# Optimization experiments

Measured on AMD Instinct MI355X. Metric: run time of the kernel, lower is better.

## Reference

```python
import jax, jax.numpy as jnp
import numpy as np

N_MOL, N_ATOM, DEG = 32, 128, 32
N = N_MOL * N_ATOM          # 4096 real atoms (no blanks)
P = N * DEG                 # 131072 pairs
N_SENS = 20
SOFT_MIN, SOFT_MAX, HARD_MAX = 0.7, 5.0, 7.5
N_IN, N_OUT, N_HIST = 2, 3, 3
NF1 = 20                    # hipnn1 n_features
NF0 = 2 * NF1               # hipnn0 n_features (doubled in __init__)
NG = 4 * NF1                # gate logits width of InteractLayer W
N_ATOM_LAYERS = 3
NIN0 = 2 + N_HIST           # one-hot over {1,8} + x_h channels


def setup_inputs():
    rng = np.random.default_rng(0)
    species = 1 + 7 * rng.integers(0, 2, size=(N_MOL, N_ATOM))  # values in {1,8}, all nonblank
    base = np.repeat(np.arange(N), DEG)
    local = base % N_ATOM
    neigh = (local + 1 + rng.integers(0, N_ATOM - 1, size=P)) % N_ATOM  # neighbor != self
    pair_second = (base // N_ATOM) * N_ATOM + neigh                     # same-molecule pairs
    key = jax.random.key(0)
    ks = jax.random.split(key, 20)
    g = lambda i, shape, s=0.1: jax.random.normal(ks[i], shape, dtype=jnp.float32) * s
    return {
        "species": jnp.asarray(species, jnp.int32),
        "coordinates": jax.random.uniform(ks[0], (N_MOL, N_ATOM, 3), jnp.float32, 0.0, 6.0),
        "x_h": g(1, (N_MOL, N_ATOM, N_HIST)),
        "x_raw": g(2, (N_MOL, N_ATOM, N_IN)),
        "pair_first": jnp.asarray(base, jnp.int32),
        "pair_second": jnp.asarray(pair_second, jnp.int32),
        "h0_int_w": g(3, (N_SENS, NIN0, NF0)),
        "h0_self_w": g(4, (NIN0, NF0)),
        "h0_self_b": g(5, (NF0,)),
        "h0_aw": g(6, (N_ATOM_LAYERS, NF0, NF0)),
        "h0_ab": g(7, (N_ATOM_LAYERS, NF0)),
        "h1_int_w": g(8, (N_SENS, 1, NF1)),
        "h1_self_w": g(9, (1, NF1)),
        "h1_self_b": g(10, (NF1,)),
        "h1_aw": g(11, (N_ATOM_LAYERS, NF1, NF1)),
        "h1_ab": g(12, (N_ATOM_LAYERS, NF1)),
        "W_int_w": g(13, (N_SENS, NF0, NG)),
        "W_self_w": g(14, (NF0, NG)),
        "W_self_b": g(15, (NG,)),
        "pw0": g(16, (NIN0, 1)),
        "pw1": g(17, (NF1, 1)),
        "pb1": g(18, (1,)),
    }


def _sensitivity(d):
    # inverse-distance gaussian sensitivities with smooth hard cutoff
    mu = jnp.linspace(1.0 / SOFT_MAX, 1.0 / SOFT_MIN, N_SENS)
    sigma = (1.0 / SOFT_MIN - 1.0 / SOFT_MAX) / N_SENS
    sense = jnp.exp(-0.5 * jnp.square((1.0 / d[:, None] - mu) / sigma))
    cut = jnp.where(d < HARD_MAX, jnp.square(jnp.cos(jnp.pi * d / (2.0 * HARD_MAX))), 0.0)
    return sense * cut[:, None]                                     # (P, n_sens)


def _interact(x, sense, pf, ps, int_w, self_w, self_b):
    # gather neighbor features, weight by sensitivities, scatter-add to center atom
    msg = sense[:, :, None] * x[ps][:, None, :]                     # (P, ns, fin)
    env = jax.ops.segment_sum(msg, pf, num_segments=N)              # (N, ns, fin)
    ns, fin, fout = int_w.shape
    return env.reshape(N, ns * fin) @ int_w.reshape(ns * fin, fout) + x @ self_w + self_b


def _hipnn(x, sense, pf, ps, int_w, self_w, self_b, aw, ab):
    y = jax.nn.softplus(_interact(x, sense, pf, ps, int_w, self_w, self_b))
    for i in range(aw.shape[0]):
        y = jax.nn.softplus(y @ aw[i] + ab[i])
    return x, y   # (input features, final block features)


def _forward(coordinates, x_h, x_raw,
             h0_int_w, h0_self_w, h0_self_b, h0_aw, h0_ab,
             h1_int_w, h1_self_w, h1_self_b, h1_aw, h1_ab,
             W_int_w, W_self_w, W_self_b, pw0, pw1, pb1,
             species, pair_first, pair_second):
    enc = (species.reshape(-1)[:, None] == jnp.array([1, 8])).astype(jnp.float32)  # OneHotSpecies
    coord = coordinates.reshape(-1, 3)
    diff = coord[pair_first] - coord[pair_second]
    d = jnp.sqrt(jnp.sum(diff * diff, axis=-1) + 1e-12)
    sense = _sensitivity(d)
    ind_f = jnp.concatenate([enc, x_h.reshape(N, N_HIST)], axis=1)  # (N, 5)
    f0_in, f0_out = _hipnn(ind_f, sense, pair_first, pair_second,
                           h0_int_w, h0_self_w, h0_self_b, h0_aw, h0_ab)
    c_t, h_t = f0_out[:, : NF0 // 2], f0_out[:, NF0 // 2:]

    def onestep(x_in, h_t, c_t):
        x_t = _hipnn(x_in, sense, pair_first, pair_second,
                     h1_int_w, h1_self_w, h1_self_b, h1_aw, h1_ab)[1]
        tmp = _interact(jnp.concatenate([x_t, h_t], axis=-1), sense,
                        pair_first, pair_second, W_int_w, W_self_w, W_self_b)
        tmp = tmp.reshape(N, NF1, 4)
        o_t = jax.nn.sigmoid(tmp[..., 3])
        c_t = jax.nn.sigmoid(tmp[..., 1]) * c_t + jax.nn.sigmoid(tmp[..., 0]) * jnp.tanh(tmp[..., 2])
        h_t = o_t * jnp.tanh(c_t)
        return o_t, h_t, c_t

    xr = x_raw.reshape(N, N_IN)
    o_t = None
    for t in range(N_IN):
        o_t, h_t, c_t = onestep(xr[:, t:t + 1], h_t, c_t)
    x0 = f0_in @ pw0 + o_t @ pw1 + pb1                              # PredictAtom
    outs = []
    for t in range(N_OUT):
        o_t, h_t, c_t = onestep(x0, h_t, c_t)
        x0 = f0_in @ pw0 + o_t @ pw1 + pb1
        outs.append(x0)
    return jnp.concatenate(outs, axis=-1)                           # (N, n_out)


def reference(species, coordinates, x_h, x_raw, pair_first, pair_second,
              h0_int_w, h0_self_w, h0_self_b, h0_aw, h0_ab,
              h1_int_w, h1_self_w, h1_self_b, h1_aw, h1_ab,
              W_int_w, W_self_w, W_self_b, pw0, pw1, pb1):
    return _forward(coordinates, x_h, x_raw,
                    h0_int_w, h0_self_w, h0_self_b, h0_aw, h0_ab,
                    h1_int_w, h1_self_w, h1_self_b, h1_aw, h1_ab,
                    W_int_w, W_self_w, W_self_b, pw0, pw1, pb1,
                    species, pair_first, pair_second)
```

## Files before the change

kernel.cpp:

```cpp
#include <hip/hip_runtime.h>
#include <hip/hip_bf16.h>


#define DEG 32
#define NA 4096
#define NP 131072

typedef __hip_bfloat16 bf16;
typedef __attribute__((ext_vector_type(8))) short short8v;
typedef __attribute__((ext_vector_type(4))) float f32x4;

#define Z0F 16.27906976744186f
#define DZ  1.0526315789473684f

__device__ __forceinline__ float frcp(float x){ return __builtin_amdgcn_rcpf(x); }
__device__ __forceinline__ float sigmoid_f(float x){ return frcp(1.f + __expf(-x)); }
__device__ __forceinline__ float tanh_f(float x){ return 1.f - 2.f*frcp(__expf(2.f*x)+1.f); }
__device__ __forceinline__ float softplus_f(float x){ return fmaxf(x,0.f) + __logf(1.f + __expf(-fabsf(x))); }
__device__ __forceinline__ unsigned bf16pack(float lo, float hi){
  unsigned ul = __float_as_uint(lo), uh = __float_as_uint(hi);
  unsigned rl = (ul + 0x7fffu + ((ul>>16)&1u)) >> 16;
  unsigned rh = (uh + 0x7fffu + ((uh>>16)&1u)) & 0xffff0000u;
  return rl | rh;
}
__device__ __forceinline__ unsigned short b16u(float v){
  unsigned u = __float_as_uint(v);
  return (unsigned short)((u + 0x7fffu + ((u>>16)&1u)) >> 16);
}
union UU { unsigned u[4]; short8v v; };
union U4 { uint4 q; short8v v; unsigned u[4]; };

__device__ __forceinline__ void wr_tile(unsigned* er, f32x4 D, int M, int N,
                                        int lg, int lr, int l){
  #pragma unroll
  for(int r=0;r<4;r++){
    float vd = D[r];
    float pr = __shfl_xor(vd, 1);
    int s = M*16 + lg*4 + r, f = N*16 + lr;
    if(!(l&1) && s<20 && f<40) er[s*20 + (f>>1)] = bf16pack(vd, pr);
  }
}

__global__ __launch_bounds__(256) void k_prep(
    const int* __restrict__ pf, const int* __restrict__ ps,
    const int* __restrict__ species,
    const float* __restrict__ coord, const float* __restrict__ xh,
    const float* __restrict__ pw0, const float* __restrict__ pb1,
    const float* __restrict__ Wint, const float* __restrict__ Wself,
    unsigned short* __restrict__ svA, unsigned* __restrict__ svB,
    unsigned* __restrict__ Amf,
    bf16* __restrict__ Wmf, float* __restrict__ indf, float* __restrict__ proj0)
{
  int b = blockIdx.x, t = threadIdx.x;
  if (b < 512){
    int p = b*256 + t;
    int i = pf[p], j = ps[p];
    float dx = coord[i*3+0]-coord[j*3+0];
    float dy = coord[i*3+1]-coord[j*3+1];
    float dz = coord[i*3+2]-coord[j*3+2];
    float d = sqrtf(dx*dx+dy*dy+dz*dz + 1e-12f);
    float cu = 0.f;
    if (d < 7.5f){ float c = __cosf(d * 0.20943951023931953f); cu = c*c; }
    float z0 = (1.f/d - 0.2f)*Z0F;
    int atom = p>>5, k = p&31;
    float sv[20], svn[20];
    #pragma unroll
    for(int s=0;s<20;s++){
      float z = z0 - (float)s*DZ;
      sv[s] = cu*__expf(-0.5f*z*z);
    }
    #pragma unroll
    for(int s=0;s<20;s++) svn[s] = __shfl_down(sv[s], 1);
    #pragma unroll
    for(int s=0;s<20;s++) svA[atom*640 + s*32 + k] = b16u(sv[s]);
    #pragma unroll
    for(int s2=0;s2<10;s2++) svB[atom*320 + k*10 + s2] = bf16pack(sv[2*s2], sv[2*s2+1]);
    if (!(k&1)){
      int lg = k>>3, q = (k>>1)&3;
      #pragma unroll
      for(int s=0;s<20;s++){
        int lr = s&15, fr = s>>4;
        Amf[atom*512 + (lg*16+lr)*8 + fr*4 + q] = bf16pack(sv[s], svn[s]);
      }
    } else {
      int idx = k>>1;
      int lg2 = idx>>2, q2 = idx&3;
      #pragma unroll
      for(int j2=0;j2<12;j2++){
        int lr = 4+j2;
        Amf[atom*512 + (lg2*16+lr)*8 + 4 + q2] = 0u;
      }
    }
  } else if (b < 782){
    int tid = (b-512)*256 + t;
    if (tid < 69120){
      int j = tid & 7, l = (tid>>3) & 63, gt = (tid>>9)%5, slab = tid/2560;
      int k = slab*32 + ((l>>4)<<3) + j;
      int g = gt*16 + (l&15);
      float v = 0.f;
      if (k < 800)      v = Wint[k*80+g];
      else if (k < 840) v = Wself[(k-800)*80+g];
      Wmf[tid] = __float2bfloat16(v);
    }
  } else {
    int tid = (b-782)*256 + t;
    if (tid < NA){
      int sp = species[tid];
      float f0 = (sp==1)?1.f:0.f, f1 = (sp==8)?1.f:0.f;
      float f2=xh[tid*3+0], f3=xh[tid*3+1], f4=xh[tid*3+2];
      indf[tid*5+0]=f0; indf[tid*5+1]=f1; indf[tid*5+2]=f2;
      indf[tid*5+3]=f3; indf[tid*5+4]=f4;
      proj0[tid] = pb1[0] + f0*pw0[0] + f1*pw0[1] + f2*pw0[2]
                 + f3*pw0[3] + f4*pw0[4];
    }
  }
}

#define F_SVT  0
#define F_INDF 10432
#define F_ENV0 11072
#define F_Y0A  12672
#define F_Y0B  13312
#define F_NB   13952
#define F_SMEM 14080
__device__ void f0_body(float* smem, int t, int mol, int sib,
    const int* __restrict__ ps, const unsigned* __restrict__ svB,
    const float* __restrict__ indf_g,
    const float* __restrict__ h0_iw, const float* __restrict__ h0_sw,
    const float* __restrict__ h0_sb, const float* __restrict__ h0_aw,
    const float* __restrict__ h0_ab,
    float* __restrict__ c_g, unsigned* __restrict__ h_p)
{
  const int nbase = mol*128;
  const int abase = nbase + sib*16;
  float* svt  = smem + F_SVT;
  float* indf = smem + F_INDF;
  float* env0 = smem + F_ENV0;
  float* y0a  = smem + F_Y0A;
  float* y0b  = smem + F_Y0B;
  unsigned char* nb8 = (unsigned char*)(smem + F_NB);

  for(int i=t;i<5120;i+=512){
    int a=i/320, q=i%320, k=q/10, s2=q%10;
    unsigned v = svB[(abase+a)*320 + q];
    float* dst = svt + a*652 + k*20 + s2*2;
    dst[0] = __uint_as_float(v<<16);
    dst[1] = __uint_as_float(v & 0xffff0000u);
  }
  for(int i=t;i<640;i+=512) indf[i] = indf_g[nbase*5 + i];
  if (t < 512) nb8[t] = (unsigned char)(ps[abase*DEG + t] - nbase);
  __syncthreads();

  for(int task=t; task<1600; task+=512){
    int a = task/100, e = task%100, s = e/5, f = e%5;
    const float* svr = svt + a*652;
    const unsigned char* nbr = nb8 + a*32;
    float acc = 0.f;
    for(int k=0;k<32;k++) acc += svr[k*20+s]*indf[nbr[k]*5+f];
    env0[a*100+e] = acc;
  }
  __syncthreads();
  for(int task=t; task<640; task+=512){
    int a=task/40, o=task%40, row=(sib*16)+a;
    float acc = h0_sb[o];
    #pragma unroll
    for(int f=0;f<5;f++) acc += indf[row*5+f]*h0_sw[f*40+o];
    for(int e=0;e<100;e++) acc += env0[a*100+e]*h0_iw[e*40+o];
    y0a[a*40+o] = softplus_f(acc);
  }
  __syncthreads();
  float* cur = y0a; float* nxt = y0b;
  for(int l=0;l<3;l++){
    for(int task=t; task<640; task+=512){
      int a=task/40, o=task%40;
      float acc = h0_ab[l*40+o];
      for(int f=0;f<40;f++) acc += cur[a*40+f]*h0_aw[l*1600+f*40+o];
      nxt[a*40+o] = softplus_f(acc);
    }
    __syncthreads();
    float* tswap=cur; cur=nxt; nxt=tswap;
  }
  if (t < 320){ int a=t/20,u=t%20; c_g[(abase+a)*20+u] = cur[a*40+u]; }
  if (t < 160){ int a=t/10,p=t%10;
    h_p[NA*10 + (abase+a)*10+p] = bf16pack(cur[a*40+20+2*p], cur[a*40+21+2*p]); }
}

#define X_XIN 0
#define X_NB  128
#define X_WTS 256
#define X_EV1 1956
#define X_YA  2276
#define X_YB  2596
__device__ void xt_body(float* smem, int t, int mol, int sib,
    const int* __restrict__ ps, const unsigned short* __restrict__ svA,
    const float* __restrict__ xraw, const float* __restrict__ x0g,
    int use_raw, int col,
    const float* __restrict__ h1_iw, const float* __restrict__ h1_sw,
    const float* __restrict__ h1_sb, const float* __restrict__ h1_aw,
    const float* __restrict__ h1_ab,
    unsigned* __restrict__ xt_p)
{
  const int nbase = mol*128;
  const int abase = nbase + sib*16;
  float* xin = smem + X_XIN;
  unsigned char* nb8 = (unsigned char*)(smem + X_NB);
  float* wts = smem + X_WTS;
  float* ev1 = smem + X_EV1;
  float* yA  = smem + X_YA;
  float* yB  = smem + X_YB;

  if (t < 128) xin[t] = use_raw ? xraw[(nbase+t)*2+col] : x0g[nbase+t];
  if (t < 512) nb8[t] = (unsigned char)(ps[abase*DEG+t] - nbase);
  for(int i=t;i<1700;i+=512){
    float v;
    if(i<400){ int o=i/20,s=i%20; v=h1_iw[s*20+o]; }
    else if(i<420) v=h1_sw[i-400];
    else if(i<440) v=h1_sb[i-420];
    else if(i<1640){ int q=i-440,L=q/400,rem=q%400,o=rem/20,f=rem%20; v=h1_aw[L*400+f*20+o]; }
    else v=h1_ab[i-1640];
    wts[i]=v;
  }
  __syncthreads();

  if (t < 320){
    int a=t/20, s=t%20;
    const uint4* sp4 = (const uint4*)(svA + (abase+a)*640 + s*32);
    const unsigned char* nbr = nb8 + a*32;
    float acc = 0.f;
    #pragma unroll
    for(int c4=0;c4<4;c4++){
      uint4 w = sp4[c4];
      unsigned wu[4] = {w.x,w.y,w.z,w.w};
      #pragma unroll
      for(int j=0;j<4;j++){
        float flo = __uint_as_float(wu[j]<<16);
        float fhi = __uint_as_float(wu[j] & 0xffff0000u);
        int k = c4*8 + 2*j;
        acc += flo*xin[nbr[k]] + fhi*xin[nbr[k+1]];
      }
    }
    ev1[t] = acc;
  }
  __syncthreads();
  if (t < 320){
    int a=t/20, o=t%20;
    float acc = wts[420+o] + xin[sib*16+a]*wts[400+o];
    const float* e = ev1 + a*20; const float* w = wts + o*20;
    #pragma unroll
    for(int s=0;s<20;s++) acc += e[s]*w[s];
    yA[t] = softplus_f(acc);
  }
  __syncthreads();
  #pragma unroll
  for(int L=0;L<2;L++){
    const float* src = (L==0)? yA : yB;
    float* dst       = (L==0)? yB : yA;
    if (t < 320){
      int a=t/20, o=t%20;
      float acc = wts[1640+L*20+o];
      const float* sr = src + a*20; const float* w = wts + 440 + L*400 + o*20;
      #pragma unroll
      for(int f=0;f<20;f++) acc += sr[f]*w[f];
      dst[t] = softplus_f(acc);
    }
    __syncthreads();
  }
  if (t < 160){
    int a=t/10, p=t%10, o0=2*p, o1=o0+1;
    const float* e = yA + a*20;
    float a0 = wts[1680+o0], a1 = wts[1680+o1];
    const float* wA = wts + 1240 + o0*20;
    const float* wB = wA + 20;
    #pragma unroll
    for(int f=0;f<20;f++){ a0 += e[f]*wA[f]; a1 += e[f]*wB[f]; }
    xt_p[(abase+a)*10+p] = bf16pack(softplus_f(a0), softplus_f(a1));
  }
}

__global__ __launch_bounds__(512) void k_fx(
    const int* __restrict__ ps, const unsigned* __restrict__ svB,
    const unsigned short* __restrict__ svA,
    const float* __restrict__ indf_g, const float* __restrict__ xraw,
    const float* __restrict__ h0_iw, const float* __restrict__ h0_sw,
    const float* __restrict__ h0_sb, const float* __restrict__ h0_aw,
    const float* __restrict__ h0_ab,
    const float* __restrict__ h1_iw, const float* __restrict__ h1_sw,
    const float* __restrict__ h1_sb, const float* __restrict__ h1_aw,
    const float* __restrict__ h1_ab,
    float* __restrict__ c_g, unsigned* __restrict__ h_p,
    unsigned* __restrict__ xt_p0, unsigned* __restrict__ xt_p1)
{
  __shared__ float smem[F_SMEM];
  const int t = threadIdx.x;
  const int sel = blockIdx.x >> 8;
  const int blk = blockIdx.x & 255;
  const int mol = blk & 31, sib = blk >> 5;
  if (sel == 0)
    f0_body(smem, t, mol, sib, ps, svB, indf_g,
            h0_iw,h0_sw,h0_sb,h0_aw,h0_ab, c_g, h_p);
  else
    xt_body(smem, t, mol, sib, ps, svA, xraw, (const float*)0, 1, sel-1,
            h1_iw,h1_sw,h1_sb,h1_aw,h1_ab, (sel==1)? xt_p0 : xt_p1);
}

__global__ __launch_bounds__(512) void k_xt(
    const int* __restrict__ ps, const unsigned short* __restrict__ svA,
    const float* __restrict__ xraw, const float* __restrict__ x0g,
    const float* __restrict__ h1_iw, const float* __restrict__ h1_sw,
    const float* __restrict__ h1_sb, const float* __restrict__ h1_aw,
    const float* __restrict__ h1_ab,
    unsigned* __restrict__ xt_p)
{
  __shared__ float smem[2916];
  const int t = threadIdx.x;
  const int mol = blockIdx.x & 31, sib = blockIdx.x >> 5;
  xt_body(smem, t, mol, sib, ps, svA, xraw, x0g, 0, 0,
          h1_iw,h1_sw,h1_sb,h1_aw,h1_ab, xt_p);
}

#define E_XHP 0
#define E_NB  2560
#define E_PRJ 2688
#define E_PW1 2704
#define E_ER  2728
#define E_TMP 9704
#define E_RED 10984
#define E_HT  11304
#define E_SMEM 11624
__global__ __launch_bounds__(512) void k_env(
    const int* __restrict__ ps, const unsigned* __restrict__ Amf,
    const unsigned* __restrict__ xt_p, const unsigned* __restrict__ h_p,
    int rpar, int wpar,
    const bf16* __restrict__ Wmf, const float* __restrict__ Wb,
    const float* __restrict__ pw1, const float* __restrict__ proj0,
    float* __restrict__ c_g, unsigned* __restrict__ h_po,
    float* __restrict__ x0g, float* __restrict__ outp, int out_col)
{
  __shared__ float smem[E_SMEM];
  const int t = threadIdx.x;
  const int mol = blockIdx.x & 31, sib = blockIdx.x >> 5;
  const int nbase = mol*128;
  const int abase = nbase + sib*16;
  unsigned* xhp = (unsigned*)(smem + E_XHP);
  unsigned char* nb8 = (unsigned char*)(smem + E_NB);
  float* prj  = smem + E_PRJ;
  float* pw1s = smem + E_PW1;
  unsigned* er = (unsigned*)(smem + E_ER);

  for(int i=t;i<1280;i+=512){
    int r=i/10, p=i%10;
    xhp[r*20+p]    = xt_p[(nbase+r)*10+p];
    xhp[r*20+10+p] = h_p[rpar*NA*10 + (nbase+r)*10+p];
  }
  if (t < 512) nb8[t] = (unsigned char)(ps[abase*DEG + t] - nbase);
  if (t < 16) prj[t] = proj0[abase+t];
  if (t < 20) pw1s[t] = pw1[t];
  __syncthreads();

  {
    const int wv = t>>6, l = t&63, lg = (t>>4)&3, lr = t&15;
    f32x4 z4 = {0.f,0.f,0.f,0.f};
    #pragma unroll
    for(int ai=0; ai<2; ++ai){
      int a = wv*2 + ai;
      int atom_g = abase + a;
      const U4* ap = (const U4*)(Amf + (unsigned)atom_g*512u + (unsigned)l*8u);
      U4 A0 = ap[0], A1 = ap[1];
      const unsigned* nbw = (const unsigned*)(nb8 + a*32 + lg*8);
      unsigned nw0=nbw[0], nw1=nbw[1];
      int nl[8];
      #pragma unroll
      for(int j2=0;j2<4;j2++){ nl[j2]=(nw0>>(8*j2))&255; nl[4+j2]=(nw1>>(8*j2))&255; }
      f32x4 d00,d01,d02,d10,d11,d12;
      {
        UU B; int f=lr; unsigned sh=(f&1)<<4;
        #pragma unroll
        for(int q=0;q<4;q++){
          unsigned wlo = xhp[nl[2*q]*20 + (f>>1)];
          unsigned whi = xhp[nl[2*q+1]*20 + (f>>1)];
          B.u[q] = ((wlo>>sh)&0xffffu) | (((whi>>sh)&0xffffu)<<16);
        }
        d00=__builtin_amdgcn_mfma_f32_16x16x32_bf16(A0.v,B.v,z4,0,0,0);
        d10=__builtin_amdgcn_mfma_f32_16x16x32_bf16(A1.v,B.v,z4,0,0,0);
      }
      {
        UU B; int f=16+lr; unsigned sh=(f&1)<<4;
        #pragma unroll
        for(int q=0;q<4;q++){
          unsigned wlo = xhp[nl[2*q]*20 + (f>>1)];
          unsigned whi = xhp[nl[2*q+1]*20 + (f>>1)];
          B.u[q] = ((wlo>>sh)&0xffffu) | (((whi>>sh)&0xffffu)<<16);
        }
        d01=__builtin_amdgcn_mfma_f32_16x16x32_bf16(A0.v,B.v,z4,0,0,0);
        d11=__builtin_amdgcn_mfma_f32_16x16x32_bf16(A1.v,B.v,z4,0,0,0);
      }
      {
        UU B; int f=32+lr; unsigned sh=(f&1)<<4; int val=(f<40);
        #pragma unroll
        for(int q=0;q<4;q++){
          if (val){
            unsigned wlo = xhp[nl[2*q]*20 + (f>>1)];
            unsigned whi = xhp[nl[2*q+1]*20 + (f>>1)];
            B.u[q] = ((wlo>>sh)&0xffffu) | (((whi>>sh)&0xffffu)<<16);
          } else B.u[q] = 0u;
        }
        d02=__builtin_amdgcn_mfma_f32_16x16x32_bf16(A0.v,B.v,z4,0,0,0);
        d12=__builtin_amdgcn_mfma_f32_16x16x32_bf16(A1.v,B.v,z4,0,0,0);
      }
      unsigned* era = er + a*436;
      wr_tile(era,d00,0,0,lg,lr,l); wr_tile(era,d01,0,1,lg,lr,l);
      wr_tile(era,d02,0,2,lg,lr,l); wr_tile(era,d10,1,0,lg,lr,l);
      wr_tile(era,d11,1,1,lg,lr,l); wr_tile(era,d12,1,2,lg,lr,l);
    }
  }
  if (t < 320){ int a=t/20, f2=t%20; er[a*436+400+f2] = xhp[(sib*16+a)*20+f2]; }
  if (t < 256) er[(t>>4)*436 + 420 + (t&15)] = 0u;
  __syncthreads();

  float* tmp_s = smem + E_TMP;
  if (t < 320){
    int wv = t >> 6, l = t & 63;
    f32x4 cacc = {0.f,0.f,0.f,0.f};
    const unsigned* abase_p = er + (l & 15)*436 + ((l>>4)<<2);
    const short8v* bptr = (const short8v*)Wmf + (wv*64 + l);
    #pragma unroll 3
    for(int slab=0; slab<27; ++slab){
      short8v av = *(const short8v*)(abase_p + slab*16);
      short8v bv = bptr[slab*320];
      cacc = __builtin_amdgcn_mfma_f32_16x16x32_bf16(av, bv, cacc, 0,0,0);
    }
    int g = wv*16 + (l & 15);
    float wb = Wb[g];
    int r0 = (l>>4)*4;
    #pragma unroll
    for(int r=0;r<4;r++) tmp_s[(r0+r)*80 + g] = cacc[r] + wb;
  }
  __syncthreads();

  float* red = smem + E_RED;
  float* ht  = smem + E_HT;
  if (t < 320){
    int a=t/20, u=t%20;
    float4 tv = *(const float4*)(tmp_s + a*80 + u*4);
    float cold = c_g[(abase+a)*20+u];
    float cnew = sigmoid_f(tv.y)*cold + sigmoid_f(tv.x)*tanh_f(tv.z);
    float og   = sigmoid_f(tv.w);
    c_g[(abase+a)*20+u] = cnew;
    ht[a*20+u]  = og*tanh_f(cnew);
    red[a*20+u] = og*pw1s[u];
  }
  __syncthreads();
  if (t < 160){
    int a=t/10, p=t%10;
    h_po[wpar*NA*10 + (abase+a)*10+p] = bf16pack(ht[a*20+2*p], ht[a*20+2*p+1]);
  }
  if (t < 16){
    float accx = prj[t];
    #pragma unroll
    for(int u=0;u<20;u++) accx += red[t*20+u];
    x0g[abase+t] = accx;
    if (out_col >= 0) outp[(abase+t)*3+out_col] = accx;
  }
}

extern "C" void kernel_launch(void* const* d_in, const int* in_sizes, int n_in,
                              void* d_out, int out_size, void* d_ws, size_t ws_size,
                              hipStream_t stream)
{
  const int*   species = (const int*)  d_in[0];
  const float* coord   = (const float*)d_in[1];
  const float* xh      = (const float*)d_in[2];
  const float* xraw    = (const float*)d_in[3];
  const int*   pf      = (const int*)  d_in[4];
  const int*   ps      = (const int*)  d_in[5];
  const float* h0_intw = (const float*)d_in[6];
  const float* h0_sw   = (const float*)d_in[7];
  const float* h0_sb   = (const float*)d_in[8];
  const float* h0_aw   = (const float*)d_in[9];
  const float* h0_ab   = (const float*)d_in[10];
  const float* h1_intw = (const float*)d_in[11];
  const float* h1_sw   = (const float*)d_in[12];
  const float* h1_sb   = (const float*)d_in[13];
  const float* h1_aw   = (const float*)d_in[14];
  const float* h1_ab   = (const float*)d_in[15];
  const float* W_intw  = (const float*)d_in[16];
  const float* W_sw    = (const float*)d_in[17];
  const float* W_sb    = (const float*)d_in[18];
  const float* pw0     = (const float*)d_in[19];
  const float* pw1     = (const float*)d_in[20];
  const float* pb1     = (const float*)d_in[21];
  float* outp = (float*)d_out;

  float* w = (float*)d_ws;
  unsigned short* svA = (unsigned short*)w;  w += NA*320;
  unsigned* svB = (unsigned*)w;              w += NA*320;
  unsigned* Amf = (unsigned*)w;              w += NA*512;
  bf16* Wmf = (bf16*)w;                      w += 34560;
  float* indf = w;                           w += NA*5;
  float* proj0 = w;                          w += NA;
  unsigned* xt_pA = (unsigned*)w;            w += NA*10;
  unsigned* xt_pB = (unsigned*)w;            w += NA*10;
  unsigned* h_p = (unsigned*)w;              w += 2*NA*10;
  float* x0g = w;                            w += NA;
  float* c_g = w;                            w += NA*20;

  k_prep<<<800,256,0,stream>>>(pf,ps,species,coord,xh,pw0,pb1,W_intw,W_sw,
                               svA,svB,Amf,Wmf,indf,proj0);
  k_fx<<<768,512,0,stream>>>(ps,svB,svA,indf,xraw,
                             h0_intw,h0_sw,h0_sb,h0_aw,h0_ab,
                             h1_intw,h1_sw,h1_sb,h1_aw,h1_ab,
                             c_g,h_p,xt_pA,xt_pB);
  for(int step=0; step<5; ++step){
    int rpar = (step+1)&1, wpar = step&1;
    int out_col = (step>=2)? (step-2) : -1;
    unsigned* xtp = (step&1)? xt_pB : xt_pA;
    if (step >= 2)
      k_xt<<<256,512,0,stream>>>(ps,svA,xraw,x0g,
                                 h1_intw,h1_sw,h1_sb,h1_aw,h1_ab, xtp);
    k_env<<<256,512,0,stream>>>(ps,Amf,xtp,h_p,rpar,wpar,
                                Wmf,W_sb,pw1,proj0,
                                c_g,h_p,x0g,outp,out_col);
  }
}
```

Before: 105.9 us.

## Fuse per-step hipnn1 feature computation into the interaction kernel

Removes the separate k_xt kernel and the xt parts of k_fx. Each k_env block now recomputes the hipnn1 features for all 128 atoms of its molecule in shared memory before the MFMA interaction stage, and k_f0 runs alone. This drops three kernel launches and the global round trip of the xt buffers. In exchange, each molecule's hipnn1 work is done redundantly by 8 blocks, and the extra shared-memory use and serial phases may lower occupancy.

```diff
diff --git a/kernel.cpp b/kernel.cpp
--- a/kernel.cpp
+++ b/kernel.cpp
@@ -123,7 +123,7 @@
 #define F_Y0B  13312
 #define F_NB   13952
 #define F_SMEM 14080
-__device__ void f0_body(float* smem, int t, int mol, int sib,
+__global__ __launch_bounds__(512) void k_f0(
     const int* __restrict__ ps, const unsigned* __restrict__ svB,
     const float* __restrict__ indf_g,
     const float* __restrict__ h0_iw, const float* __restrict__ h0_sw,
@@ -131,6 +131,9 @@
     const float* __restrict__ h0_ab,
     float* __restrict__ c_g, unsigned* __restrict__ h_p)
 {
+  __shared__ float smem[F_SMEM];
+  const int t = threadIdx.x;
+  const int mol = blockIdx.x & 31, sib = blockIdx.x >> 5;
   const int nbase = mol*128;
   const int abase = nbase + sib*16;
   float* svt  = smem + F_SVT;
@@ -185,152 +188,29 @@
     h_p[NA*10 + (abase+a)*10+p] = bf16pack(cur[a*40+20+2*p], cur[a*40+21+2*p]); }
 }
 
-#define X_XIN 0
-#define X_NB  128
-#define X_WTS 256
-#define X_EV1 1956
-#define X_YA  2276
-#define X_YB  2596
-__device__ void xt_body(float* smem, int t, int mol, int sib,
+#define E_XHP 0
+#define E_NB  2560
+#define E_XIN 3584
+#define E_PRJ 3712
+#define E_PW1 3728
+#define E_AR  3752
+#define E_WTS E_AR
+#define E_EV1 (E_AR+1700)
+#define E_YA  (E_AR+4260)
+#define E_ER  E_AR
+#define E_TMP (E_AR+6976)
+#define E_RED (E_AR+8256)
+#define E_HT  (E_AR+8576)
+#define E_SMEM (E_AR+8896)
+__global__ __launch_bounds__(512) void k_env(
     const int* __restrict__ ps, const unsigned short* __restrict__ svA,
-    const float* __restrict__ xraw, const float* __restrict__ x0g,
+    const unsigned* __restrict__ Amf,
+    const float* __restrict__ xraw, const float* __restrict__ x0g_in,
     int use_raw, int col,
     const float* __restrict__ h1_iw, const float* __restrict__ h1_sw,
     const float* __restrict__ h1_sb, const float* __restrict__ h1_aw,
     const float* __restrict__ h1_ab,
-    unsigned* __restrict__ xt_p)
-{
-  const int nbase = mol*128;
-  const int abase = nbase + sib*16;
-  float* xin = smem + X_XIN;
-  unsigned char* nb8 = (unsigned char*)(smem + X_NB);
-  float* wts = smem + X_WTS;
-  float* ev1 = smem + X_EV1;
-  float* yA  = smem + X_YA;
-  float* yB  = smem + X_YB;
-
-  if (t < 128) xin[t] = use_raw ? xraw[(nbase+t)*2+col] : x0g[nbase+t];
-  if (t < 512) nb8[t] = (unsigned char)(ps[abase*DEG+t] - nbase);
-  for(int i=t;i<1700;i+=512){
-    float v;
-    if(i<400){ int o=i/20,s=i%20; v=h1_iw[s*20+o]; }
-    else if(i<420) v=h1_sw[i-400];
-    else if(i<440) v=h1_sb[i-420];
-    else if(i<1640){ int q=i-440,L=q/400,rem=q%400,o=rem/20,f=rem%20; v=h1_aw[L*400+f*20+o]; }
-    else v=h1_ab[i-1640];
-    wts[i]=v;
-  }
-  __syncthreads();
-
-  if (t < 320){
-    int a=t/20, s=t%20;
-    const uint4* sp4 = (const uint4*)(svA + (abase+a)*640 + s*32);
-    const unsigned char* nbr = nb8 + a*32;
-    float acc = 0.f;
-    #pragma unroll
-    for(int c4=0;c4<4;c4++){
-      uint4 w = sp4[c4];
-      unsigned wu[4] = {w.x,w.y,w.z,w.w};
-      #pragma unroll
-      for(int j=0;j<4;j++){
-        float flo = __uint_as_float(wu[j]<<16);
-        float fhi = __uint_as_float(wu[j] & 0xffff0000u);
-        int k = c4*8 + 2*j;
-        acc += flo*xin[nbr[k]] + fhi*xin[nbr[k+1]];
-      }
-    }
-    ev1[t] = acc;
-  }
-  __syncthreads();
-  if (t < 320){
-    int a=t/20, o=t%20;
-    float acc = wts[420+o] + xin[sib*16+a]*wts[400+o];
-    const float* e = ev1 + a*20; const float* w = wts + o*20;
-    #pragma unroll
-    for(int s=0;s<20;s++) acc += e[s]*w[s];
-    yA[t] = softplus_f(acc);
-  }
-  __syncthreads();
-  #pragma unroll
-  for(int L=0;L<2;L++){
-    const float* src = (L==0)? yA : yB;
-    float* dst       = (L==0)? yB : yA;
-    if (t < 320){
-      int a=t/20, o=t%20;
-      float acc = wts[1640+L*20+o];
-      const float* sr = src + a*20; const float* w = wts + 440 + L*400 + o*20;
-      #pragma unroll
-      for(int f=0;f<20;f++) acc += sr[f]*w[f];
-      dst[t] = softplus_f(acc);
-    }
-    __syncthreads();
-  }
-  if (t < 160){
-    int a=t/10, p=t%10, o0=2*p, o1=o0+1;
-    const float* e = yA + a*20;
-    float a0 = wts[1680+o0], a1 = wts[1680+o1];
-    const float* wA = wts + 1240 + o0*20;
-    const float* wB = wA + 20;
-    #pragma unroll
-    for(int f=0;f<20;f++){ a0 += e[f]*wA[f]; a1 += e[f]*wB[f]; }
-    xt_p[(abase+a)*10+p] = bf16pack(softplus_f(a0), softplus_f(a1));
-  }
-}
-
-__global__ __launch_bounds__(512) void k_fx(
-    const int* __restrict__ ps, const unsigned* __restrict__ svB,
-    const unsigned short* __restrict__ svA,
-    const float* __restrict__ indf_g, const float* __restrict__ xraw,
-    const float* __restrict__ h0_iw, const float* __restrict__ h0_sw,
-    const float* __restrict__ h0_sb, const float* __restrict__ h0_aw,
-    const float* __restrict__ h0_ab,
-    const float* __restrict__ h1_iw, const float* __restrict__ h1_sw,
-    const float* __restrict__ h1_sb, const float* __restrict__ h1_aw,
-    const float* __restrict__ h1_ab,
-    float* __restrict__ c_g, unsigned* __restrict__ h_p,
-    unsigned* __restrict__ xt_p0, unsigned* __restrict__ xt_p1)
-{
-  __shared__ float smem[F_SMEM];
-  const int t = threadIdx.x;
-  const int sel = blockIdx.x >> 8;
-  const int blk = blockIdx.x & 255;
-  const int mol = blk & 31, sib = blk >> 5;
-  if (sel == 0)
-    f0_body(smem, t, mol, sib, ps, svB, indf_g,
-            h0_iw,h0_sw,h0_sb,h0_aw,h0_ab, c_g, h_p);
-  else
-    xt_body(smem, t, mol, sib, ps, svA, xraw, (const float*)0, 1, sel-1,
-            h1_iw,h1_sw,h1_sb,h1_aw,h1_ab, (sel==1)? xt_p0 : xt_p1);
-}
-
-__global__ __launch_bounds__(512) void k_xt(
-    const int* __restrict__ ps, const unsigned short* __restrict__ svA,
-    const float* __restrict__ xraw, const float* __restrict__ x0g,
-    const float* __restrict__ h1_iw, const float* __restrict__ h1_sw,
-    const float* __restrict__ h1_sb, const float* __restrict__ h1_aw,
-    const float* __restrict__ h1_ab,
-    unsigned* __restrict__ xt_p)
-{
-  __shared__ float smem[2916];
-  const int t = threadIdx.x;
-  const int mol = blockIdx.x & 31, sib = blockIdx.x >> 5;
-  xt_body(smem, t, mol, sib, ps, svA, xraw, x0g, 0, 0,
-          h1_iw,h1_sw,h1_sb,h1_aw,h1_ab, xt_p);
-}
-
-#define E_XHP 0
-#define E_NB  2560
-#define E_PRJ 2688
-#define E_PW1 2704
-#define E_ER  2728
-#define E_TMP 9704
-#define E_RED 10984
-#define E_HT  11304
-#define E_SMEM 11624
-__global__ __launch_bounds__(512) void k_env(
-    const int* __restrict__ ps, const unsigned* __restrict__ Amf,
-    const unsigned* __restrict__ xt_p, const unsigned* __restrict__ h_p,
-    int rpar, int wpar,
+    const unsigned* __restrict__ h_p, int rpar, int wpar,
     const bf16* __restrict__ Wmf, const float* __restrict__ Wb,
     const float* __restrict__ pw1, const float* __restrict__ proj0,
     float* __restrict__ c_g, unsigned* __restrict__ h_po,
@@ -343,30 +223,99 @@
   const int abase = nbase + sib*16;
   unsigned* xhp = (unsigned*)(smem + E_XHP);
   unsigned char* nb8 = (unsigned char*)(smem + E_NB);
+  float* xin  = smem + E_XIN;
   float* prj  = smem + E_PRJ;
   float* pw1s = smem + E_PW1;
-  unsigned* er = (unsigned*)(smem + E_ER);
+  float* wts  = smem + E_WTS;
+  float* ev1  = smem + E_EV1;
+  float* yA   = smem + E_YA;
 
   for(int i=t;i<1280;i+=512){
     int r=i/10, p=i%10;
-    xhp[r*20+p]    = xt_p[(nbase+r)*10+p];
     xhp[r*20+10+p] = h_p[rpar*NA*10 + (nbase+r)*10+p];
   }
-  if (t < 512) nb8[t] = (unsigned char)(ps[abase*DEG + t] - nbase);
+  for(int i=t;i<4096;i+=512) nb8[i] = (unsigned char)(ps[nbase*DEG+i] - nbase);
+  if (t < 128) xin[t] = use_raw ? xraw[(nbase+t)*2+col] : x0g_in[nbase+t];
+  for(int i=t;i<1700;i+=512){
+    float v;
+    if(i<400){ int o=i/20,s=i%20; v=h1_iw[s*20+o]; }
+    else if(i<420) v=h1_sw[i-400];
+    else if(i<440) v=h1_sb[i-420];
+    else if(i<1640){ int q=i-440,L=q/400,rem=q%400,o=rem/20,f=rem%20; v=h1_aw[L*400+f*20+o]; }
+    else v=h1_ab[i-1640];
+    wts[i]=v;
+  }
   if (t < 16) prj[t] = proj0[abase+t];
   if (t < 20) pw1s[t] = pw1[t];
   __syncthreads();
 
+  for(int task=t; task<2560; task+=512){
+    int r=task/20, s=task%20;
+    const uint4* sp4 = (const uint4*)(svA + (nbase+r)*640 + s*32);
+    const unsigned char* nbr = nb8 + r*32;
+    float acc = 0.f;
+    #pragma unroll
+    for(int c4=0;c4<4;c4++){
+      uint4 w = sp4[c4];
+      unsigned wu[4] = {w.x,w.y,w.z,w.w};
+      #pragma unroll
+      for(int j=0;j<4;j++){
+        float flo = __uint_as_float(wu[j]<<16);
+        float fhi = __uint_as_float(wu[j] & 0xffff0000u);
+        int k = c4*8 + 2*j;
+        acc += flo*xin[nbr[k]] + fhi*xin[nbr[k+1]];
+      }
+    }
+    ev1[r*20+s] = acc;
+  }
+  __syncthreads();
+  for(int task=t; task<2560; task+=512){
+    int r=task/20, o=task%20;
+    float acc = wts[420+o] + xin[r]*wts[400+o];
+    const float* e = ev1 + r*20; const float* w = wts + o*20;
+    #pragma unroll
+    for(int s=0;s<20;s++) acc += e[s]*w[s];
+    yA[r*20+o] = softplus_f(acc);
+  }
+  __syncthreads();
+  #pragma unroll
+  for(int L=0;L<2;L++){
+    const float* src = (L==0)? yA : ev1;
+    float* dst       = (L==0)? ev1 : yA;
+    for(int task=t; task<2560; task+=512){
+      int r=task/20, o=task%20;
+      float acc = wts[1640+L*20+o];
+      const float* sr = src + r*20; const float* w = wts + 440 + L*400 + o*20;
+      #pragma unroll
+      for(int f=0;f<20;f++) acc += sr[f]*w[f];
+      dst[r*20+o] = softplus_f(acc);
+    }
+    __syncthreads();
+  }
+  for(int task=t; task<1280; task+=512){
+    int r=task/10, p=task%10, o0=2*p, o1=o0+1;
+    const float* e = yA + r*20;
+    float a0 = wts[1680+o0], a1 = wts[1680+o1];
+    const float* wA = wts + 1240 + o0*20;
+    const float* wB = wA + 20;
+    #pragma unroll
+    for(int f=0;f<20;f++){ a0 += e[f]*wA[f]; a1 += e[f]*wB[f]; }
+    xhp[r*20+p] = bf16pack(softplus_f(a0), softplus_f(a1));
+  }
+  __syncthreads();
+
+  unsigned* er = (unsigned*)(smem + E_ER);
   {
     const int wv = t>>6, l = t&63, lg = (t>>4)&3, lr = t&15;
     f32x4 z4 = {0.f,0.f,0.f,0.f};
     #pragma unroll
     for(int ai=0; ai<2; ++ai){
       int a = wv*2 + ai;
+      int a_own = sib*16 + a;
       int atom_g = abase + a;
       const U4* ap = (const U4*)(Amf + (unsigned)atom_g*512u + (unsigned)l*8u);
       U4 A0 = ap[0], A1 = ap[1];
-      const unsigned* nbw = (const unsigned*)(nb8 + a*32 + lg*8);
+      const unsigned* nbw = (const unsigned*)(nb8 + a_own*32 + lg*8);
       unsigned nw0=nbw[0], nw1=nbw[1];
       int nl[8];
       #pragma unroll
@@ -498,26 +447,21 @@
   bf16* Wmf = (bf16*)w;                      w += 34560;
   float* indf = w;                           w += NA*5;
   float* proj0 = w;                          w += NA;
-  unsigned* xt_pA = (unsigned*)w;            w += NA*10;
-  unsigned* xt_pB = (unsigned*)w;            w += NA*10;
   unsigned* h_p = (unsigned*)w;              w += 2*NA*10;
   float* x0g = w;                            w += NA;
   float* c_g = w;                            w += NA*20;
 
   k_prep<<<800,256,0,stream>>>(pf,ps,species,coord,xh,pw0,pb1,W_intw,W_sw,
                                svA,svB,Amf,Wmf,indf,proj0);
-  k_fx<<<768,512,0,stream>>>(ps,svB,svA,indf,xraw,
-                             h0_intw,h0_sw,h0_sb,h0_aw,h0_ab,
-                             h1_intw,h1_sw,h1_sb,h1_aw,h1_ab,
-                             c_g,h_p,xt_pA,xt_pB);
+  k_f0<<<256,512,0,stream>>>(ps,svB,indf,h0_intw,h0_sw,h0_sb,h0_aw,h0_ab,
+                             c_g,h_p);
   for(int step=0; step<5; ++step){
+    int use_raw = (step<2)?1:0, col = (step<2)? step : 0;
     int rpar = (step+1)&1, wpar = step&1;
     int out_col = (step>=2)? (step-2) : -1;
-    unsigned* xtp = (step&1)? xt_pB : xt_pA;
-    if (step >= 2)
-      k_xt<<<256,512,0,stream>>>(ps,svA,xraw,x0g,
-                                 h1_intw,h1_sw,h1_sb,h1_aw,h1_ab, xtp);
-    k_env<<<256,512,0,stream>>>(ps,Amf,xtp,h_p,rpar,wpar,
+    k_env<<<256,512,0,stream>>>(ps,svA,Amf,xraw,x0g,use_raw,col,
+                                h1_intw,h1_sw,h1_sb,h1_aw,h1_ab,
+                                h_p,rpar,wpar,
                                 Wmf,W_sb,pw1,proj0,
                                 c_g,h_p,x0g,outp,out_col);
   }
```

After: 131.9 us. 1.25x slower.
